# Performance work log

Hardware: AMD Instinct MI355X
Metric: run time of the kernel (lower is better)

The kernel has to match this reference:

```python
import jax, jax.numpy as jnp
import numpy as np

THETA_BASE = 10000.0


def _rope_tables(head_dim, seq_len):
    # intended math of precompute_rope_params (source has an arange typo;
    # standard RoPE: inv_freq over even indices)
    inv_freq = 1.0 / (THETA_BASE ** (jnp.arange(0, head_dim, 2, dtype=jnp.float32) / head_dim))
    pos = jnp.arange(seq_len, dtype=jnp.float32)
    angles = pos[:, None] * inv_freq[None, :]          # [S, hd/2]
    angles = jnp.concatenate([angles, angles], axis=1)  # [S, hd]
    return jnp.cos(angles), jnp.sin(angles)


def _apply_rope(x, cos, sin):
    # x: [B, H, S, hd]; cos/sin: [S, hd] broadcast over batch/heads
    hd = x.shape[-1]
    x1, x2 = x[..., : hd // 2], x[..., hd // 2 :]
    rotated = jnp.concatenate([-x2, x1], axis=-1)
    return x * cos + rotated * sin


def setup_inputs() -> dict:
    key = jax.random.key(0)
    ks = jax.random.split(key, 5)
    b, s, d = 2, 2048, 1024
    x = jax.random.normal(ks[0], (b, s, d), dtype=jnp.float32)
    # store weights as [d_in, d_out] so y = x @ W (equivalent math to nn.Linear)
    scale = 1.0 / np.sqrt(d)
    W_q = jax.random.normal(ks[1], (d, d), dtype=jnp.float32) * scale
    W_k = jax.random.normal(ks[2], (d, d), dtype=jnp.float32) * scale
    W_v = jax.random.normal(ks[3], (d, d), dtype=jnp.float32) * scale
    W_o = jax.random.normal(ks[4], (d, d), dtype=jnp.float32) * scale
    return {"x": x, "W_q": W_q, "W_k": W_k, "W_v": W_v, "W_o": W_o}


def reference(x, W_q, W_k, W_v, W_o):
    num_heads = 16
    b, s, d_in = x.shape
    d_out = W_q.shape[1]
    hd = d_out // num_heads

    def split_heads(t):  # [B,S,D] -> [B,H,S,hd]
        return t.reshape(b, s, num_heads, hd).transpose(0, 2, 1, 3)

    q = split_heads(x @ W_q)
    k = split_heads(x @ W_k)
    v = split_heads(x @ W_v)

    cos, sin = _rope_tables(hd, s)
    q = _apply_rope(q, cos, sin)
    k = _apply_rope(k, cos, sin)

    scores = jnp.einsum("bhqd,bhkd->bhqk", q, k)
    causal = jnp.triu(jnp.ones((s, s), dtype=bool), k=1)  # True above diagonal
    scores = jnp.where(causal, -jnp.inf, scores)
    attn = jax.nn.softmax(scores / jnp.sqrt(jnp.float32(hd)), axis=-1)

    ctx = jnp.einsum("bhqk,bhkd->bhqd", attn, v)
    ctx = ctx.transpose(0, 2, 1, 3).reshape(b, s, d_out)
    return ctx @ W_o
```

## Files before the change

### kernel.cpp

```cpp
#include <hip/hip_runtime.h>

typedef __bf16 bf16x8 __attribute__((ext_vector_type(8)));
typedef float f32x4 __attribute__((ext_vector_type(4)));
typedef unsigned short u16;

__device__ __forceinline__ u16 f2bf(float f){
  union { float fp; unsigned int u; } v; v.fp = f;
  unsigned int r = v.u + 0x7fffu + ((v.u >> 16) & 1u);
  return (u16)(r >> 16);
}

__device__ __forceinline__ unsigned pk2(float a, float b){
  union { float f; unsigned u; } ua, ub; ua.f = a; ub.f = b;
  return __builtin_amdgcn_perm(ub.u, ua.u, 0x07060302u);
}

__device__ __forceinline__ void glds16(const void* g, void* l){
  __builtin_amdgcn_global_load_lds((__attribute__((address_space(1))) void*)(void*)(g),
                                   (__attribute__((address_space(3))) void*)(l), 16, 0, 0);
}

__global__ __launch_bounds__(256) void prep_k(const float* __restrict__ x,
                                              const float* __restrict__ W0, const float* __restrict__ W1,
                                              const float* __restrict__ W2, const float* __restrict__ W3,
                                              u16* __restrict__ XB, u16* __restrict__ Wt,
                                              float* __restrict__ cosT, float* __restrict__ sinT){
  const int b = blockIdx.x, tid = threadIdx.x;
  if (b < 512){
    for (int i = b*256 + tid; i < (1<<20); i += 512*256){
      float4 v = ((const float4*)x)[i];
      ushort4 o;
      o.x = f2bf(v.x); o.y = f2bf(v.y); o.z = f2bf(v.z); o.w = f2bf(v.w);
      ((ushort4*)XB)[i] = o;
    }
  } else if (b < 4608){
    __shared__ float tile[32][33];
    const int b2 = b - 512;
    const int bz = b2>>10, by = (b2>>5)&31, bx = b2&31;
    const float* W = (bz==0)?W0:(bz==1)?W1:(bz==2)?W2:W3;
    u16* dst = Wt + ((size_t)bz<<20);
    const int tx = tid&31, ty = tid>>5;
    const int xx = bx*32 + tx;
    const int y0 = by*32;
    #pragma unroll
    for (int i=0;i<32;i+=8) tile[ty+i][tx] = W[(size_t)(y0+ty+i)*1024 + xx];
    __syncthreads();
    const int xo = y0 + tx;
    #pragma unroll
    for (int i=0;i<32;i+=8) dst[(size_t)(bx*32+ty+i)*1024 + xo] = f2bf(tile[tx][ty+i]);
  } else {
    const int i = (b-4608)*256 + tid;
    const int si = i>>6, dd = i&63, f = dd&31;
    float invf = exp2f(-13.287712379549449f * (float)f * (1.0f/32.0f));
    float ang = (float)si * invf;
    float s, c;
    sincosf(ang, &s, &c);
    cosT[i] = c; sinT[i] = s;
  }
}

__global__ __launch_bounds__(256,3) void gemm_qkv_k(const u16* __restrict__ xb, const u16* __restrict__ Wt,
                                                  const float* __restrict__ cosT, const float* __restrict__ sinT,
                                                  u16* __restrict__ Qr, u16* __restrict__ Kr, u16* __restrict__ Vt){
  __shared__ __align__(16) u16 As[2*128*32];
  __shared__ __align__(16) u16 Bs[2*128*32];
  const int tid = threadIdx.x;
  const int w = tid>>6, lane = tid&63, quad = lane>>4, l15 = lane&15;
  const int wrow = w>>1, wcol = w&1;
  const int m0 = blockIdx.x*128;
  const int nG0 = blockIdx.y*128;
  const int which = nG0>>10, n0 = nG0&1023;
  const u16* __restrict__ B = Wt + ((size_t)which<<20);
  f32x4 acc[4][4] = {};
  const int r4 = lane>>2, c4 = (lane&3)*8;

  for (int kb=0; kb<1024; kb+=64){
    #pragma unroll
    for (int kh=0; kh<2; kh++){
      glds16(&xb[(size_t)(m0+32*w+r4)*1024    + kb + kh*32 + c4], &As[kh*4096 + (32*w)*32]);
      glds16(&xb[(size_t)(m0+32*w+16+r4)*1024 + kb + kh*32 + c4], &As[kh*4096 + (32*w+16)*32]);
      glds16(&B [(size_t)(n0+32*w+r4)*1024    + kb + kh*32 + c4], &Bs[kh*4096 + (32*w)*32]);
      glds16(&B [(size_t)(n0+32*w+16+r4)*1024 + kb + kh*32 + c4], &Bs[kh*4096 + (32*w+16)*32]);
    }
    __syncthreads();
    bf16x8 a[4][2], b[4][2];
    #pragma unroll
    for (int t=0;t<4;t++)
      #pragma unroll
      for (int kh=0;kh<2;kh++){
        a[t][kh] = *(const bf16x8*)&As[kh*4096 + (64*wrow + 16*t + l15)*32 + quad*8];
        b[t][kh] = *(const bf16x8*)&Bs[kh*4096 + (64*wcol + 16*t + l15)*32 + quad*8];
      }
    #pragma unroll
    for (int kh=0;kh<2;kh++)
      #pragma unroll
      for (int ti=0;ti<4;ti++)
        #pragma unroll
        for (int tj=0;tj<4;tj++)
          acc[ti][tj] = __builtin_amdgcn_mfma_f32_16x16x32_bf16(a[ti][kh], b[tj][kh], acc[ti][tj], 0,0,0);
    __syncthreads();
  }

  const int colbase = n0 + 64*wcol;
  const int hh = colbase>>6;
  const int rowbase = m0 + 64*wrow + 4*quad;
  const float QSCALE = 0.18033688011112042f;

  if (which < 2){
    u16* __restrict__ out = (which==0) ? Qr : Kr;
    const float osc = (which==0) ? QSCALE : 1.0f;
    u16* __restrict__ EP = (w<2) ? &As[w*4096] : &Bs[(w-2)*4096];
    #pragma unroll
    for (int tj=0;tj<4;tj++){
      int dd = 16*tj + l15;
      int co = (dd>>5)*512 + ((dd>>3)&3)*128 + (dd&7);
      float sgn = (tj<2) ? -1.0f : 1.0f;
      int pj = tj^2;
      #pragma unroll
      for (int ti=0;ti<4;ti++){
        #pragma unroll
        for (int r=0;r<4;r++){
          int m = rowbase + 16*ti + r;
          int si = m&2047;
          float cs = cosT[(si<<6)+dd];
          float sn = sinT[(si<<6)+dd];
          float vv = (acc[ti][tj][r]*cs + sgn*acc[ti][pj][r]*sn) * osc;
          EP[ti*1024 + co + (4*quad+r)*8] = f2bf(vv);
        }
      }
    }
    #pragma unroll
    for (int ti=0;ti<4;ti++){
      int mbase = m0 + 64*wrow + 16*ti;
      int bi = mbase>>11, si16 = (mbase&2047)>>4;
      size_t gb = ((size_t)(bi*16+hh)<<17) + (size_t)si16*1024;
      #pragma unroll
      for (int g=0; g<2; g++){
        uint4 vvv = *(const uint4*)&EP[ti*1024 + g*512 + lane*8];
        *(uint4*)&out[gb + g*512 + lane*8] = vvv;
      }
    }
  } else {
    #pragma unroll
    for (int tj=0;tj<4;tj++){
      #pragma unroll
      for (int ti=0;ti<4;ti++){
        int m = rowbase + 16*ti;
        int bi = m>>11, si = m&2047;
        ushort4 pk;
        pk.x = f2bf(acc[ti][tj][0]); pk.y = f2bf(acc[ti][tj][1]);
        pk.z = f2bf(acc[ti][tj][2]); pk.w = f2bf(acc[ti][tj][3]);
        *(ushort4*)&Vt[((size_t)(bi*16+hh)<<17) + (si>>6)*4096 + ((si>>5)&1)*2048
                       + tj*512 + ((si>>3)&3)*128 + l15*8 + (si&7)] = pk;
      }
    }
  }
}

__global__ __launch_bounds__(256,3) void attn_k(const u16* __restrict__ QF, const u16* __restrict__ KF,
                                                const u16* __restrict__ VF, u16* __restrict__ ctx){
  __shared__ __align__(16) u16 SC[4*4608];
  __shared__ float LL[4][32];
  const int tid = threadIdx.x;
  const int w = tid>>6, lane = tid&63, quad = lane>>4, l15 = lane&15;
  const int Lin = blockIdx.x;
  const int xcd = Lin & 7, slot = Lin >> 3;
  const int bh = (xcd<<2) | (slot>>5);
  const int p = slot & 31;
  const u16* __restrict__ Qb = QF + ((size_t)bh<<17);
  const u16* __restrict__ Kb = KF + ((size_t)bh<<17);
  const u16* __restrict__ Vb = VF + ((size_t)bh<<17);
  u16* __restrict__ Pw = SC + w*4608;
  const int loff = lane*8;
  const int bi = bh>>4, hh = bh&15;

  #pragma unroll 1
  for (int ph=0; ph<2; ph++){
    if (ph) __syncthreads();
    const int tile = ph ? (63-p) : p;
    const int q0 = tile*32;
    const int nk = (tile>>1) + 1;

    bf16x8 qf[2][2];
    #pragma unroll
    for (int ti=0;ti<2;ti++)
      #pragma unroll
      for (int kh=0;kh<2;kh++)
        qf[ti][kh] = *(const bf16x8*)&Qb[(2*tile+ti)*1024 + kh*512 + loff];

    f32x4 o[2][4] = {};
    float ls[2] = {0.f, 0.f};

    for (int kt = w; kt < nk; kt += 4){
      const int k0 = kt*64;
      bf16x8 kf[4][2], vf[4][2];
      #pragma unroll
      for (int tjk=0;tjk<4;tjk++)
        #pragma unroll
        for (int kh=0;kh<2;kh++)
          kf[tjk][kh] = *(const bf16x8*)&Kb[(4*kt+tjk)*1024 + kh*512 + loff];
      #pragma unroll
      for (int tjd=0;tjd<4;tjd++)
        #pragma unroll
        for (int kh=0;kh<2;kh++)
          vf[tjd][kh] = *(const bf16x8*)&Vb[kt*4096 + kh*2048 + tjd*512 + loff];

      f32x4 st[2][4] = {};
      #pragma unroll
      for (int ti=0;ti<2;ti++)
        #pragma unroll
        for (int tjk=0;tjk<4;tjk++){
          st[ti][tjk] = __builtin_amdgcn_mfma_f32_16x16x32_bf16(kf[tjk][0], qf[ti][0], st[ti][tjk], 0,0,0);
          st[ti][tjk] = __builtin_amdgcn_mfma_f32_16x16x32_bf16(kf[tjk][1], qf[ti][1], st[ti][tjk], 0,0,0);
        }

      #pragma unroll
      for (int ti=0;ti<2;ti++){
        const int qbase = q0 + 16*ti;
        f32x4 pv[4];
        if (k0 + 63 > qbase){
          const int qg = qbase + l15;
          #pragma unroll
          for (int tjk=0;tjk<4;tjk++)
            #pragma unroll
            for (int r=0;r<4;r++){
              int kg = k0 + 16*tjk + 4*quad + r;
              pv[tjk][r] = (kg > qg) ? 0.0f : exp2f(st[ti][tjk][r]);
            }
        } else {
          #pragma unroll
          for (int tjk=0;tjk<4;tjk++)
            #pragma unroll
            for (int r=0;r<4;r++)
              pv[tjk][r] = exp2f(st[ti][tjk][r]);
        }
        f32x4 t4 = (pv[0]+pv[1]) + (pv[2]+pv[3]);
        float rs = (t4[0]+t4[1]) + (t4[2]+t4[3]);
        rs += __shfl_xor(rs, 16, 64);
        rs += __shfl_xor(rs, 32, 64);
        ls[ti] += rs;
        #pragma unroll
        for (int tjk=0;tjk<4;tjk++){
          uint2 pk;
          pk.x = pk2(pv[tjk][0], pv[tjk][1]);
          pk.y = pk2(pv[tjk][2], pv[tjk][3]);
          *(uint2*)&Pw[(16*ti + l15)*72 + 16*tjk + 4*quad] = pk;
        }
      }

      bf16x8 pf[2][2];
      #pragma unroll
      for (int ti=0;ti<2;ti++)
        #pragma unroll
        for (int kh=0;kh<2;kh++)
          pf[ti][kh] = *(const bf16x8*)&Pw[(16*ti + l15)*72 + 32*kh + quad*8];
      #pragma unroll
      for (int ti=0;ti<2;ti++)
        #pragma unroll
        for (int tjd=0;tjd<4;tjd++){
          o[ti][tjd] = __builtin_amdgcn_mfma_f32_16x16x32_bf16(pf[ti][0], vf[tjd][0], o[ti][tjd], 0,0,0);
          o[ti][tjd] = __builtin_amdgcn_mfma_f32_16x16x32_bf16(pf[ti][1], vf[tjd][1], o[ti][tjd], 0,0,0);
        }
    }

    float* __restrict__ Ob = (float*)&SC[w*4608];
    #pragma unroll
    for (int ti=0;ti<2;ti++)
      #pragma unroll
      for (int tjd=0;tjd<4;tjd++)
        *(f32x4*)&Ob[(16*tjd + l15)*36 + 16*ti + 4*quad] = o[ti][tjd];
    if (quad == 0){
      LL[w][l15]      = ls[0];
      LL[w][16 + l15] = ls[1];
    }
    __syncthreads();

    #pragma unroll
    for (int ti=0;ti<2;ti++){
      f32x4 om = {0.f,0.f,0.f,0.f};
      #pragma unroll
      for (int w2=0;w2<4;w2++)
        om += *(const f32x4*)&((const float*)&SC[w2*4608])[(16*w + l15)*36 + 16*ti + 4*quad];
      #pragma unroll
      for (int r=0;r<4;r++){
        int ridx = 16*ti + 4*quad + r;
        float lv = LL[0][ridx] + LL[1][ridx] + LL[2][ridx] + LL[3][ridx];
        int sq = q0 + ridx;
        ctx[(((size_t)(bi*2048 + sq))<<10) + (hh<<6) + 16*w + l15] = f2bf(om[r] / lv);
      }
    }
  }
}

__global__ __launch_bounds__(256,3) void gemm_out_k(const u16* __restrict__ cb, const u16* __restrict__ Wot,
                                                  float* __restrict__ out){
  __shared__ __align__(16) u16 As[2*64*32];
  __shared__ __align__(16) u16 Bs[2*128*32];
  const int tid = threadIdx.x;
  const int w = tid>>6, lane = tid&63, quad = lane>>4, l15 = lane&15;
  const int wrow = w>>1, wcol = w&1;
  const int m0 = blockIdx.x*64;
  const int nG0 = blockIdx.y*128;
  f32x4 acc[2][4] = {};
  const int r4 = lane>>2, c4 = (lane&3)*8;

  for (int kb=0; kb<1024; kb+=64){
    #pragma unroll
    for (int kh=0; kh<2; kh++){
      glds16(&cb [(size_t)(m0+16*w+r4)*1024     + kb + kh*32 + c4], &As[kh*2048 + (16*w)*32]);
      glds16(&Wot[(size_t)(nG0+32*w+r4)*1024    + kb + kh*32 + c4], &Bs[kh*4096 + (32*w)*32]);
      glds16(&Wot[(size_t)(nG0+32*w+16+r4)*1024 + kb + kh*32 + c4], &Bs[kh*4096 + (32*w+16)*32]);
    }
    __syncthreads();
    bf16x8 a[2][2], b[4][2];
    #pragma unroll
    for (int kh=0;kh<2;kh++){
      #pragma unroll
      for (int t=0;t<2;t++)
        a[t][kh] = *(const bf16x8*)&As[kh*2048 + (32*wrow + 16*t + l15)*32 + quad*8];
      #pragma unroll
      for (int t=0;t<4;t++)
        b[t][kh] = *(const bf16x8*)&Bs[kh*4096 + (64*wcol + 16*t + l15)*32 + quad*8];
    }
    #pragma unroll
    for (int kh=0;kh<2;kh++)
      #pragma unroll
      for (int ti=0;ti<2;ti++)
        #pragma unroll
        for (int tj=0;tj<4;tj++)
          acc[ti][tj] = __builtin_amdgcn_mfma_f32_16x16x32_bf16(a[ti][kh], b[tj][kh], acc[ti][tj], 0,0,0);
    __syncthreads();
  }

  const int rowbase = m0 + 32*wrow + 4*quad;
  const int colb = nG0 + 64*wcol;
  #pragma unroll
  for (int ti=0;ti<2;ti++){
    #pragma unroll
    for (int r=0;r<4;r++){
      int m = rowbase + 16*ti + r;
      float* orow = out + (size_t)m*1024 + colb;
      #pragma unroll
      for (int tj=0;tj<4;tj++)
        orow[16*tj + l15] = acc[ti][tj][r];
    }
  }
}

extern "C" void kernel_launch(void* const* d_in, const int* in_sizes, int n_in,
                              void* d_out, int out_size, void* d_ws, size_t ws_size,
                              hipStream_t stream){
  const float* x  = (const float*)d_in[0];
  const float* Wq = (const float*)d_in[1];
  const float* Wk = (const float*)d_in[2];
  const float* Wv = (const float*)d_in[3];
  const float* Wo = (const float*)d_in[4];
  float* out = (float*)d_out;
  u16* ws = (u16*)d_ws;

  u16* XB  = ws;
  u16* WT  = ws + ((size_t)4<<20);
  u16* QFp = ws + ((size_t)8<<20);
  u16* KFp = ws + ((size_t)12<<20);
  u16* VFp = ws + ((size_t)16<<20);
  u16* CTX = ws + ((size_t)20<<20);
  float* COS = (float*)(ws + ((size_t)24<<20));
  float* SIN = COS + (1<<17);

  prep_k       <<<5120, 256, 0, stream>>>(x, Wq, Wk, Wv, Wo, XB, WT, COS, SIN);
  gemm_qkv_k   <<<dim3(32,24), 256, 0, stream>>>(XB, WT, COS, SIN, QFp, KFp, VFp);
  attn_k       <<<1024, 256, 0, stream>>>(QFp, KFp, VFp, CTX);
  gemm_out_k   <<<dim3(64,8), 256, 0, stream>>>(CTX, WT + ((size_t)3<<20), out);
}
```

Baseline: 175.0 us.

## Stream K fragments per 16-key subtile to cut registers and raise occupancy

Restructures the attention inner loop so each 16-key subtile's K fragment is loaded (with one-step prefetch), scored, exponentiated and written to LDS in a rolled loop, instead of holding all four K fragments and the full score tile in registers. Row-sum cross-lane shuffles move out of the key loop and run once per phase. Launch bounds go from 3 to 4 blocks per CU. The aim is lower VGPR pressure for higher occupancy and fewer shuffles. In exchange, the rolled loops reduce instruction-level parallelism and the overlap of MFMAs with global loads.

```diff
diff --git a/kernel.cpp b/kernel.cpp
--- a/kernel.cpp
+++ b/kernel.cpp
@@ -157,7 +157,7 @@
   }
 }
 
-__global__ __launch_bounds__(256,3) void attn_k(const u16* __restrict__ QF, const u16* __restrict__ KF,
+__global__ __launch_bounds__(256,4) void attn_k(const u16* __restrict__ QF, const u16* __restrict__ KF,
                                                 const u16* __restrict__ VF, u16* __restrict__ ctx){
   __shared__ __align__(16) u16 SC[4*4608];
   __shared__ float LL[4][32];
@@ -191,60 +191,48 @@
     f32x4 o[2][4] = {};
     float ls[2] = {0.f, 0.f};
 
+    #pragma unroll 1
     for (int kt = w; kt < nk; kt += 4){
       const int k0 = kt*64;
-      bf16x8 kf[4][2], vf[4][2];
-      #pragma unroll
-      for (int tjk=0;tjk<4;tjk++)
-        #pragma unroll
-        for (int kh=0;kh<2;kh++)
-          kf[tjk][kh] = *(const bf16x8*)&Kb[(4*kt+tjk)*1024 + kh*512 + loff];
+      bf16x8 vf[4][2];
       #pragma unroll
       for (int tjd=0;tjd<4;tjd++)
         #pragma unroll
         for (int kh=0;kh<2;kh++)
           vf[tjd][kh] = *(const bf16x8*)&Vb[kt*4096 + kh*2048 + tjd*512 + loff];
 
-      f32x4 st[2][4] = {};
-      #pragma unroll
-      for (int ti=0;ti<2;ti++)
-        #pragma unroll
-        for (int tjk=0;tjk<4;tjk++){
-          st[ti][tjk] = __builtin_amdgcn_mfma_f32_16x16x32_bf16(kf[tjk][0], qf[ti][0], st[ti][tjk], 0,0,0);
-          st[ti][tjk] = __builtin_amdgcn_mfma_f32_16x16x32_bf16(kf[tjk][1], qf[ti][1], st[ti][tjk], 0,0,0);
+      bf16x8 kfn0 = *(const bf16x8*)&Kb[(4*kt)*1024 + loff];
+      bf16x8 kfn1 = *(const bf16x8*)&Kb[(4*kt)*1024 + 512 + loff];
+      #pragma unroll 1
+      for (int tjk=0;tjk<4;tjk++){
+        bf16x8 kf0 = kfn0, kf1 = kfn1;
+        if (tjk < 3){
+          kfn0 = *(const bf16x8*)&Kb[(4*kt+tjk+1)*1024 + loff];
+          kfn1 = *(const bf16x8*)&Kb[(4*kt+tjk+1)*1024 + 512 + loff];
         }
-
-      #pragma unroll
-      for (int ti=0;ti<2;ti++){
-        const int qbase = q0 + 16*ti;
-        f32x4 pv[4];
-        if (k0 + 63 > qbase){
-          const int qg = qbase + l15;
-          #pragma unroll
-          for (int tjk=0;tjk<4;tjk++)
+        #pragma unroll
+        for (int ti=0;ti<2;ti++){
+          f32x4 st = {0.f,0.f,0.f,0.f};
+          st = __builtin_amdgcn_mfma_f32_16x16x32_bf16(kf0, qf[ti][0], st, 0,0,0);
+          st = __builtin_amdgcn_mfma_f32_16x16x32_bf16(kf1, qf[ti][1], st, 0,0,0);
+          f32x4 pv;
+          const int qbase = q0 + 16*ti;
+          if (k0 + 16*tjk + 15 > qbase){
+            const int qg = qbase + l15;
             #pragma unroll
             for (int r=0;r<4;r++){
               int kg = k0 + 16*tjk + 4*quad + r;
-              pv[tjk][r] = (kg > qg) ? 0.0f : exp2f(st[ti][tjk][r]);
+              pv[r] = (kg > qg) ? 0.0f : exp2f(st[r]);
             }
-        } else {
-          #pragma unroll
-          for (int tjk=0;tjk<4;tjk++)
+          } else {
             #pragma unroll
-            for (int r=0;r<4;r++)
-              pv[tjk][r] = exp2f(st[ti][tjk][r]);
-        }
-        f32x4 t4 = (pv[0]+pv[1]) + (pv[2]+pv[3]);
-        float rs = (t4[0]+t4[1]) + (t4[2]+t4[3]);
-        rs += __shfl_xor(rs, 16, 64);
-        rs += __shfl_xor(rs, 32, 64);
-        ls[ti] += rs;
-        #pragma unroll
-        for (int tjk=0;tjk<4;tjk++){
-          uint2 pk;
-          pk.x = pk2(pv[tjk][0], pv[tjk][1]);
-          pk.y = pk2(pv[tjk][2], pv[tjk][3]);
-          *(uint2*)&Pw[(16*ti + l15)*72 + 16*tjk + 4*quad] = pk;
+            for (int r=0;r<4;r++) pv[r] = exp2f(st[r]);
+          }
+          ls[ti] += (pv[0]+pv[1]) + (pv[2]+pv[3]);
+          uint2 pk_;
+          pk_.x = pk2(pv[0], pv[1]);
+          pk_.y = pk2(pv[2], pv[3]);
+          *(uint2*)&Pw[(16*ti + l15)*72 + 16*tjk + 4*quad] = pk_;
         }
       }
 
@@ -261,6 +249,14 @@
           o[ti][tjd] = __builtin_amdgcn_mfma_f32_16x16x32_bf16(pf[ti][0], vf[tjd][0], o[ti][tjd], 0,0,0);
           o[ti][tjd] = __builtin_amdgcn_mfma_f32_16x16x32_bf16(pf[ti][1], vf[tjd][1], o[ti][tjd], 0,0,0);
         }
+    }
+
+    #pragma unroll
+    for (int ti=0;ti<2;ti++){
+      float rs = ls[ti];
+      rs += __shfl_xor(rs, 16, 64);
+      rs += __shfl_xor(rs, 32, 64);
+      ls[ti] = rs;
     }
 
     float* __restrict__ Ob = (float*)&SC[w*4608];
```

Result: no change. 177.4 us (+1.4%).
